# Kernel optimization log

Measured on AMD Instinct MI355X. Metric: run time of the kernel, lower is better.

The kernel has to match this reference:

```python
import jax, jax.numpy as jnp
import numpy as np

EMBED_DIM = 512
NUM_HEADS = 8
HEAD_DIM = EMBED_DIM // NUM_HEADS
B, N, M = 4, 4096, 4096


def setup_inputs() -> dict:
    key = jax.random.key(0)
    ks = jax.random.split(key, 16)
    s = 0.02
    inp = {
        "query": jax.random.normal(ks[0], (B, N, EMBED_DIM), jnp.float32),
        "key": jax.random.normal(ks[1], (B, M, EMBED_DIM), jnp.float32),
        "value": jax.random.normal(ks[2], (B, M, EMBED_DIM), jnp.float32),
        # Linear weights stored as (in, out) so y = x @ W + b (== torch x @ W.T + b)
        "Wq": jax.random.normal(ks[3], (EMBED_DIM, EMBED_DIM), jnp.float32) * s,
        "bq": jnp.zeros((EMBED_DIM,), jnp.float32),
        "Wk": jax.random.normal(ks[4], (EMBED_DIM, EMBED_DIM), jnp.float32) * s,
        "bk": jnp.zeros((EMBED_DIM,), jnp.float32),
        "Wv": jax.random.normal(ks[5], (EMBED_DIM, EMBED_DIM), jnp.float32) * s,
        "bv": jnp.zeros((EMBED_DIM,), jnp.float32),
        # rank expansion MLP acts per-head on head_dim
        "W1": jax.random.normal(ks[6], (HEAD_DIM, HEAD_DIM * 2), jnp.float32) * s,
        "b1": jnp.zeros((HEAD_DIM * 2,), jnp.float32),
        "W2": jax.random.normal(ks[7], (HEAD_DIM * 2, HEAD_DIM), jnp.float32) * s,
        "b2": jnp.zeros((HEAD_DIM,), jnp.float32),
        "Wo": jax.random.normal(ks[8], (EMBED_DIM, EMBED_DIM), jnp.float32) * s,
        "bo": jnp.zeros((EMBED_DIM,), jnp.float32),
    }
    return inp


def reference(query, key, value, Wq, bq, Wk, bk, Wv, bv, W1, b1, W2, b2, Wo, bo):
    b, n, _ = query.shape
    m = key.shape[1]
    H, D = NUM_HEADS, HEAD_DIM
    # ELU+1 feature maps on projected q, k
    q = jax.nn.elu(query @ Wq + bq) + 1.0           # [B,N,E]
    k = jax.nn.elu(key @ Wk + bk) + 1.0             # [B,M,E]
    v = value @ Wv + bv                              # [B,M,E]
    q = q.reshape(b, n, H, D)
    k = k.reshape(b, m, H, D)
    v = v.reshape(b, m, H, D)
    # rank expansion MLP on keys (per head_dim), exact GELU as nn.GELU default
    k_aug = jax.nn.gelu(k @ W1 + b1, approximate=False) @ W2 + b2
    k_aug = jax.nn.elu(k_aug) + 1.0                  # [B,M,H,D]
    # inputs already fp32 (torch .float() casts are identity here)
    k_scaled = k_aug / m                             # normalize over context len
    kv_context = jnp.einsum('bmhd,bmhe->bhde', k_scaled, v)   # [B,H,D,D]
    out = jnp.einsum('bnhd,bhde->bnhe', q, kv_context)        # [B,N,H,D]
    k_sum = k_scaled.sum(axis=1)                      # [B,H,D]
    denom = jnp.einsum('bnhd,bhd->bnh', q, k_sum)     # [B,N,H]
    out = out / jnp.clip(denom, 1e-6, None)[..., None]
    out = jnp.clip(jnp.nan_to_num(out, nan=0.0, posinf=65000.0, neginf=-65000.0),
                   -65000.0, 65000.0)
    out = out.reshape(b, n, H * D)
    return out @ Wo + bo
```

## Files before the change

kernel.cpp:

```cpp
#include <hip/hip_runtime.h>
#include <hip/hip_bf16.h>
#include <cmath>

#define DEV __device__ __forceinline__

typedef __bf16 bf16x8 __attribute__((ext_vector_type(8)));
typedef float f32x4 __attribute__((ext_vector_type(4)));
typedef unsigned int u32;
typedef unsigned short u16;

#define S_VMCNT(N) asm volatile("s_waitcnt vmcnt(" #N ")" ::: "memory")
#define S_LGKM0    asm volatile("s_waitcnt lgkmcnt(0)" ::: "memory")
#define S_FENCE    asm volatile("" ::: "memory")
#define S_BAR      __builtin_amdgcn_s_barrier()

DEV u16 f2bf(float f) {
  union { float f; u32 u; } v;
  v.f = f;
  u32 u = v.u;
  u += 0x7fffu + ((u >> 16) & 1u);
  return (u16)(u >> 16);
}
DEV u32 pk2(float a, float b) {
  union { __hip_bfloat162 h2; u32 u; } v;
  v.h2 = __float22bfloat162_rn(float2{a, b});
  return v.u;
}

DEV void async16(const void* g, void* l) {
  __builtin_amdgcn_global_load_lds((const __attribute__((address_space(1))) u32*)g,
                                   (__attribute__((address_space(3))) u32*)l, 16, 0, 0);
}

DEV int swz(int row, int kq) { return row * 64 + ((kq * 8) ^ ((row & 7) << 3)); }

__global__ __launch_bounds__(256, 2)
void qkv_gemm(const float* __restrict__ qin, const float* __restrict__ kin,
              const float* __restrict__ vin, const u16* __restrict__ WqP,
              const u16* __restrict__ WkP, const u16* __restrict__ WvP,
              const float* __restrict__ bq, const float* __restrict__ bk,
              const float* __restrict__ bv, const u16* __restrict__ W1T,
              const u16* __restrict__ W2T, const float* __restrict__ b1,
              const float* __restrict__ b2, u16* __restrict__ qact,
              u16* __restrict__ vT, u16* __restrict__ kaT, float invM)
{
  __shared__ __align__(16) u16 SB[32768];

  const int z = blockIdx.z;
  const float* Af = z == 0 ? qin : z == 1 ? kin : vin;
  const u16* Bp = z == 0 ? WqP : z == 1 ? WkP : WvP;
  const float* bias = z == 0 ? bq : z == 1 ? bk : bv;

  const int tid = threadIdx.x, wv = tid >> 6, lane = tid & 63;
  const int wr = wv >> 1, wc = wv & 1;
  const int lrow = lane & 15, lq = lane >> 4;
  const long r0 = (long)blockIdx.x * 128;
  const int c0 = blockIdx.y * 128;

  f32x4 acc[4][4] = {};
  float4 rA[2][8];

  auto loadA = [&](float4* dst, int T) {
#pragma unroll
    for (int it = 0; it < 4; ++it) {
      const int s = it * 256 + tid;
      const int row = s >> 3, kq = s & 7;
      const float* g = Af + (r0 + row) * 512 + T * 64 + kq * 8;
      dst[2 * it]     = *(const float4*)g;
      dst[2 * it + 1] = *(const float4*)(g + 4);
    }
  };
  auto cvtStoreA = [&](const float4* src, u16* bufA) {
#pragma unroll
    for (int it = 0; it < 4; ++it) {
      const int s = it * 256 + tid;
      const int row = s >> 3, kq = s & 7;
      union { u32 q[4]; uint4 v; } pk;
      pk.q[0] = pk2(src[2 * it].x, src[2 * it].y);
      pk.q[1] = pk2(src[2 * it].z, src[2 * it].w);
      pk.q[2] = pk2(src[2 * it + 1].x, src[2 * it + 1].y);
      pk.q[3] = pk2(src[2 * it + 1].z, src[2 * it + 1].w);
      *(uint4*)&bufA[swz(row, kq)] = pk.v;
    }
  };
  auto issueB = [&](int T, u16* bufB) {
#pragma unroll
    for (int it = 0; it < 4; ++it) {
      const int sl = it * 256 + wv * 64;
      async16(Bp + ((long)blockIdx.y * 8 + T) * 8192 + (sl + lane) * 8, &bufB[sl * 8]);
    }
  };
  auto computeT = [&](const u16* Ac, const u16* Bc) {
#pragma unroll
    for (int subk = 0; subk < 2; ++subk) {
      bf16x8 af[4], bfr[4];
#pragma unroll
      for (int i = 0; i < 4; ++i)
        af[i] = *(const bf16x8*)&Ac[swz(wr * 64 + i * 16 + lrow, subk * 4 + lq)];
#pragma unroll
      for (int j = 0; j < 4; ++j)
        bfr[j] = *(const bf16x8*)&Bc[swz(wc * 64 + j * 16 + lrow, subk * 4 + lq)];
#pragma unroll
      for (int i = 0; i < 4; ++i)
#pragma unroll
        for (int j = 0; j < 4; ++j)
          acc[i][j] = __builtin_amdgcn_mfma_f32_16x16x32_bf16(af[i], bfr[j], acc[i][j], 0, 0, 0);
    }
  };

  issueB(0, SB + 8192);
  S_FENCE;
  loadA(rA[0], 0);
  loadA(rA[1], 1);
  cvtStoreA(rA[0], SB);
  S_LGKM0;
  S_VMCNT(8);
  S_BAR;

#pragma unroll
  for (int t = 0; t < 8; ++t) {
    const int cur = t & 1, nxt = 1 - cur;
    u16* Ac = SB + cur * 16384;
    u16* Bc = Ac + 8192;
    u16* An = SB + nxt * 16384;
    u16* Bn = An + 8192;
    if (t < 7) issueB(t + 1, Bn);
    S_FENCE;
    if (t < 6) loadA(rA[cur], t + 2);
    if (t < 7) cvtStoreA(rA[nxt], An);
    computeT(Ac, Bc);
    S_LGKM0;
    if (t < 6)       { S_VMCNT(8); }
    else if (t == 6) { S_VMCNT(0); }
    S_BAR;
  }

  if (z == 0) {
#pragma unroll
    for (int i = 0; i < 4; ++i) {
#pragma unroll
      for (int j = 0; j < 4; ++j) {
        const int col = c0 + wc * 64 + j * 16 + lrow;
        const float bvv = bias[col];
#pragma unroll
        for (int p = 0; p < 4; ++p) {
          float o = acc[i][j][p] + bvv;
          o = (o > 0.f) ? (o + 1.f) : __expf(o);
          const long row = r0 + wr * 64 + i * 16 + lq * 4 + p;
          qact[row * 512 + col] = f2bf(o);
        }
      }
    }
  } else if (z == 2) {
    __syncthreads();
    u16* LTv = SB + wv * 4608;
#pragma unroll
    for (int i = 0; i < 4; ++i) {
#pragma unroll
      for (int j = 0; j < 4; ++j) {
        const int col = c0 + wc * 64 + j * 16 + lrow;
        const float bvv = bias[col];
        ushort4 w;
        w.x = f2bf(acc[i][j][0] + bvv);
        w.y = f2bf(acc[i][j][1] + bvv);
        w.z = f2bf(acc[i][j][2] + bvv);
        w.w = f2bf(acc[i][j][3] + bvv);
        *(ushort4*)&LTv[(j * 16 + lrow) * 72 + i * 16 + lq * 4] = w;
      }
    }
    const int b = (int)(r0 >> 12);
    const int h = (c0 + wc * 64) >> 6;
    const int mg0 = (int)(r0 & 4095) + wr * 64;
    __syncthreads();
#pragma unroll
    for (int ps = 0; ps < 8; ++ps) {
      const int e = ps * 8 + (lane >> 3);
      const int mq = (lane & 7) * 8;
      uint4 v = *(const uint4*)&LTv[e * 72 + mq];
      *(uint4*)(vT + (((long)b * 8 + h) * 64 + e) * 4096 + mg0 + mq) = v;
    }
  } else {
    u16* As_k = SB;
    u16* W1p  = SB + 9216;
    u16* W2p  = SB + 18432;
    u16* hid  = SB;
    u16* LT2  = SB;
    const int b   = (int)(r0 >> 12);
    const int m0g = (int)(r0 & 4095);
    const int h0  = c0 >> 6;
    __syncthreads();

    for (int hh = 0; hh < 2; ++hh) {
#pragma unroll
      for (int i = 0; i < 4; ++i) {
        const int c = i * 256 + tid;
        *(uint4*)&W1p[(c >> 3) * 72 + (c & 7) * 8] = *(const uint4*)(W1T + c * 8);
      }
#pragma unroll
      for (int i = 0; i < 4; ++i) {
        const int c = i * 256 + tid;
        *(uint4*)&W2p[(c >> 4) * 136 + (c & 15) * 8] = *(const uint4*)(W2T + c * 8);
      }
      if (wc == hh) {
#pragma unroll
        for (int i = 0; i < 4; ++i)
#pragma unroll
          for (int j = 0; j < 4; ++j) {
            const int col = c0 + wc * 64 + j * 16 + lrow;
            const float bvv = bias[col];
            const int d = j * 16 + lrow;
            const int mb = wr * 64 + i * 16 + lq * 4;
#pragma unroll
            for (int p = 0; p < 4; ++p) {
              float o = acc[i][j][p] + bvv;
              o = (o > 0.f) ? (o + 1.f) : __expf(o);
              As_k[(mb + p) * 72 + d] = f2bf(o);
            }
          }
      }
      __syncthreads();

      const int c0m = (wv >> 1) * 64, mh0 = (wv & 1) * 64;
      f32x4 acc1[4][4] = {};
#pragma unroll
      for (int kt = 0; kt < 2; ++kt) {
        bf16x8 wa[4], kb[4];
#pragma unroll
        for (int i = 0; i < 4; ++i)
          wa[i] = *(const bf16x8*)&W1p[(c0m + i * 16 + lrow) * 72 + kt * 32 + lq * 8];
#pragma unroll
        for (int j = 0; j < 4; ++j)
          kb[j] = *(const bf16x8*)&As_k[(mh0 + j * 16 + lrow) * 72 + kt * 32 + lq * 8];
#pragma unroll
        for (int i = 0; i < 4; ++i)
#pragma unroll
          for (int j = 0; j < 4; ++j)
            acc1[i][j] = __builtin_amdgcn_mfma_f32_16x16x32_bf16(wa[i], kb[j], acc1[i][j], 0, 0, 0);
      }
      __syncthreads();

#pragma unroll
      for (int i = 0; i < 4; ++i) {
        const int cc = c0m + i * 16 + lq * 4;
        float4 bv4 = *(const float4*)(b1 + cc);
#pragma unroll
        for (int j = 0; j < 4; ++j) {
          const int m = mh0 + j * 16 + lrow;
          float x0 = acc1[i][j][0] + bv4.x, x1 = acc1[i][j][1] + bv4.y;
          float x2 = acc1[i][j][2] + bv4.z, x3 = acc1[i][j][3] + bv4.w;
          ushort4 w;
          w.x = f2bf(0.5f * x0 * (1.f + erff(x0 * 0.7071067811865475f)));
          w.y = f2bf(0.5f * x1 * (1.f + erff(x1 * 0.7071067811865475f)));
          w.z = f2bf(0.5f * x2 * (1.f + erff(x2 * 0.7071067811865475f)));
          w.w = f2bf(0.5f * x3 * (1.f + erff(x3 * 0.7071067811865475f)));
          *(ushort4*)&hid[m * 136 + cc] = w;
        }
      }
      __syncthreads();

      const int d0 = (wv >> 1) * 32, mh2 = (wv & 1) * 64;
      f32x4 acc2[4][2] = {};
#pragma unroll
      for (int kt = 0; kt < 4; ++kt) {
        bf16x8 wa2[2], hb[4];
#pragma unroll
        for (int i = 0; i < 2; ++i)
          wa2[i] = *(const bf16x8*)&W2p[(d0 + i * 16 + lrow) * 136 + kt * 32 + lq * 8];
#pragma unroll
        for (int j = 0; j < 4; ++j)
          hb[j] = *(const bf16x8*)&hid[(mh2 + j * 16 + lrow) * 136 + kt * 32 + lq * 8];
#pragma unroll
        for (int j = 0; j < 4; ++j)
#pragma unroll
          for (int i = 0; i < 2; ++i)
            acc2[j][i] = __builtin_amdgcn_mfma_f32_16x16x32_bf16(hb[j], wa2[i], acc2[j][i], 0, 0, 0);
      }
      __syncthreads();

#pragma unroll
      for (int i = 0; i < 2; ++i) {
        const int d = d0 + i * 16 + lrow;
        const float bd = b2[d];
#pragma unroll
        for (int j = 0; j < 4; ++j) {
          const int ml = mh2 + j * 16 + lq * 4;
          ushort4 w;
#pragma unroll
          for (int p = 0; p < 4; ++p) {
            float v = acc2[j][i][p] + bd;
            v = ((v > 0.f) ? (v + 1.f) : __expf(v)) * invM;
            ((u16*)&w)[p] = f2bf(v);
          }
          *(ushort4*)&LT2[d * 136 + ml] = w;
        }
      }
      __syncthreads();

      const int bh2 = b * 8 + h0 + hh;
#pragma unroll
      for (int it = 0; it < 4; ++it) {
        const int c = it * 256 + tid;
        const int d = c >> 4, mq = (c & 15) * 8;
        uint4 v = *(const uint4*)&LT2[d * 136 + mq];
        *(uint4*)(kaT + ((long)bh2 * 64 + d) * 4096 + m0g + mq) = v;
      }
      __syncthreads();
    }
  }
}

__global__ __launch_bounds__(256, 2)
void out_gemm(const u16* __restrict__ A, const u16* __restrict__ Bt,
              const float* __restrict__ bias, float* __restrict__ Y)
{
  __shared__ __align__(16) u16 SB[32768];
  const int tid = threadIdx.x, wv = tid >> 6, lane = tid & 63;
  const int wr = wv >> 1, wc = wv & 1;
  const int lrow = lane & 15, lq = lane >> 4;
  const long r0 = (long)blockIdx.x * 128;
  const int c0 = blockIdx.y * 128;

  auto stage = [&](int T, u16* buf) {
#pragma unroll
    for (int it = 0; it < 4; ++it) {
      const int sl = it * 256 + wv * 64;
      async16(A  + ((long)blockIdx.x * 8 + T) * 8192 + (sl + lane) * 8, &buf[sl * 8]);
      async16(Bt + ((long)blockIdx.y * 8 + T) * 8192 + (sl + lane) * 8, &buf[8192 + sl * 8]);
    }
  };

  f32x4 acc[4][4] = {};
  stage(0, SB);
  S_VMCNT(0);
  S_BAR;

#pragma unroll
  for (int t = 0; t < 8; ++t) {
    const int cur = t & 1, nxt = 1 - cur;
    if (t < 7) stage(t + 1, SB + nxt * 16384);
    const u16* Ac = SB + cur * 16384;
    const u16* Bc = Ac + 8192;
#pragma unroll
    for (int subk = 0; subk < 2; ++subk) {
      bf16x8 af[4], bfr[4];
#pragma unroll
      for (int i = 0; i < 4; ++i)
        af[i] = *(const bf16x8*)&Ac[swz(wr * 64 + i * 16 + lrow, subk * 4 + lq)];
#pragma unroll
      for (int j = 0; j < 4; ++j)
        bfr[j] = *(const bf16x8*)&Bc[swz(wc * 64 + j * 16 + lrow, subk * 4 + lq)];
#pragma unroll
      for (int i = 0; i < 4; ++i)
#pragma unroll
        for (int j = 0; j < 4; ++j)
          acc[i][j] = __builtin_amdgcn_mfma_f32_16x16x32_bf16(af[i], bfr[j], acc[i][j], 0, 0, 0);
    }
    S_LGKM0;
    if (t < 7) { S_VMCNT(0); }
    S_BAR;
  }
#pragma unroll
  for (int i = 0; i < 4; ++i) {
#pragma unroll
    for (int j = 0; j < 4; ++j) {
      const int col = c0 + wc * 64 + j * 16 + lrow;
      const float bv = bias[col];
#pragma unroll
      for (int p = 0; p < 4; ++p) {
        const long row = r0 + wr * 64 + i * 16 + lq * 4 + p;
        Y[row * 512 + col] = acc[i][j][p] + bv;
      }
    }
  }
}

struct TArgs {
  const float* src[6];
  u16* dst[6];
  int K[6];
  int N[6];
};
__global__ __launch_bounds__(256)
void transpose_w(TArgs a)
{
  const int m = blockIdx.z;
  const int K = a.K[m], N = a.N[m];
  const int kt = blockIdx.y * 64, nt = blockIdx.x * 64;
  if (kt >= K || nt >= N) return;
  const float* src = a.src[m];
  u16* dst = a.dst[m];
  __shared__ u16 t[64][72];
  const int tx = threadIdx.x & 15, ty = threadIdx.x >> 4;
#pragma unroll
  for (int rr = 0; rr < 64; rr += 16) {
    const int k = kt + ty + rr;
    float4 v = *(const float4*)(src + (long)k * N + nt + tx * 4);
    t[tx * 4 + 0][ty + rr] = f2bf(v.x);
    t[tx * 4 + 1][ty + rr] = f2bf(v.y);
    t[tx * 4 + 2][ty + rr] = f2bf(v.z);
    t[tx * 4 + 3][ty + rr] = f2bf(v.w);
  }
  __syncthreads();
  if (m < 4) {
    const int ktile = kt >> 6;
#pragma unroll
    for (int it = 0; it < 2; ++it) {
      const int s = threadIdx.x + it * 256;
      const int r = s >> 3, c = (s & 7) * 8;
      const int n = nt + r;
      const int colblk = n >> 7, cl = n & 127;
      ushort4 u0 = *(ushort4*)&t[r][c];
      ushort4 u1 = *(ushort4*)&t[r][c + 4];
      u16* d = dst + ((long)colblk * 8 + ktile) * 8192 + cl * 64 + (c ^ ((cl & 7) << 3));
      *(ushort4*)d = u0;
      *(ushort4*)(d + 4) = u1;
    }
  } else {
#pragma unroll
    for (int it = 0; it < 2; ++it) {
      const int s = threadIdx.x + it * 256;
      const int r = s >> 3, c = (s & 7) * 8;
      ushort4 u0 = *(ushort4*)&t[r][c];
      ushort4 u1 = *(ushort4*)&t[r][c + 4];
      *(ushort4*)(dst + (long)(nt + r) * K + kt + c) = u0;
      *(ushort4*)(dst + (long)(nt + r) * K + kt + c + 4) = u1;
    }
  }
}

__global__ __launch_bounds__(256, 2)
void kv_gemm(const u16* __restrict__ kaT, const u16* __restrict__ vT,
             float* __restrict__ kvp, float* __restrict__ ksp)
{
  const int sp = blockIdx.x;
  const int bh = blockIdx.y;
  __shared__ __align__(16) u16 SB[32768];
  const int tid = threadIdx.x, wv = tid >> 6, lane = tid & 63;
  const int lrow = lane & 15, lq = lane >> 4;
  f32x4 acc[4][4] = {};
  f32x4 accs[4] = {};
  bf16x8 ones;
#pragma unroll
  for (int z = 0; z < 8; ++z) ones[z] = (__bf16)1.0f;
  const long base = (long)bh * 64 * 4096;

#pragma unroll
  for (int ph = 0; ph < 2; ++ph) {
    const int m0 = sp * 256 + ph * 128;
#pragma unroll
    for (int i = 0; i < 4; ++i) {
      const int s = (wv * 4 + i) * 64 + lane;
      const int chunk = s >> 8, row = (s >> 2) & 63, part = s & 3;
      const long g = base + (long)row * 4096 + m0 + chunk * 32 + part * 8;
      async16(kaT + g, &SB[ph * 16384 + (wv * 4 + i) * 512]);
      async16(vT + g, &SB[ph * 16384 + 8192 + (wv * 4 + i) * 512]);
    }
    S_FENCE;
  }

#pragma unroll
  for (int ph = 0; ph < 2; ++ph) {
    if (ph == 0) { S_VMCNT(8); } else { S_VMCNT(0); }
    const u16* As = SB + ph * 16384;
    const u16* Bs = As + 8192;
    bf16x8 af[4], bfr[4];
#pragma unroll
    for (int i = 0; i < 4; ++i)
      af[i] = *(const bf16x8*)&As[wv * 2048 + (i * 16 + lrow) * 32 + lq * 8];
#pragma unroll
    for (int j = 0; j < 4; ++j)
      bfr[j] = *(const bf16x8*)&Bs[wv * 2048 + (j * 16 + lrow) * 32 + lq * 8];
#pragma unroll
    for (int i = 0; i < 4; ++i) {
#pragma unroll
      for (int j = 0; j < 4; ++j)
        acc[i][j] = __builtin_amdgcn_mfma_f32_16x16x32_bf16(af[i], bfr[j], acc[i][j], 0, 0, 0);
      accs[i] = __builtin_amdgcn_mfma_f32_16x16x32_bf16(af[i], ones, accs[i], 0, 0, 0);
    }
  }

  float* red = (float*)SB;
  float* ksr = red + 64 * 68;
  for (int w = 0; w < 4; ++w) {
    __syncthreads();
    if (wv == w) {
#pragma unroll
      for (int i = 0; i < 4; ++i) {
#pragma unroll
        for (int j = 0; j < 4; ++j) {
          const int e = j * 16 + lrow, dd = i * 16 + lq * 4;
          float* p = &red[e * 68 + dd];
          if (w == 0) { p[0] = acc[i][j][0]; p[1] = acc[i][j][1]; p[2] = acc[i][j][2]; p[3] = acc[i][j][3]; }
          else        { p[0] += acc[i][j][0]; p[1] += acc[i][j][1]; p[2] += acc[i][j][2]; p[3] += acc[i][j][3]; }
        }
        if (lrow == 0) {
          const int dd = i * 16 + lq * 4;
#pragma unroll
          for (int p2 = 0; p2 < 4; ++p2) {
            if (w == 0) ksr[dd + p2] = accs[i][p2];
            else        ksr[dd + p2] += accs[i][p2];
          }
        }
      }
    }
  }
  __syncthreads();
  float* kvo = kvp + ((long)sp * 32 + bh) * 4096;
  for (int s = tid; s < 4096; s += 256) kvo[s] = red[(s >> 6) * 68 + (s & 63)];
  if (tid < 64) ksp[(sp * 32 + bh) * 64 + tid] = ksr[tid];
}

__global__ __launch_bounds__(256)
void kv_reduce(const float* __restrict__ kvp, const float* __restrict__ ksp,
               u16* __restrict__ kvT, u16* __restrict__ ksumT)
{
  const int bh = blockIdx.x;
  const int t = threadIdx.x;
  const int s0 = blockIdx.y * 512;
#pragma unroll
  for (int i = 0; i < 2; ++i) {
    const int s = s0 + i * 256 + t;
    float v = 0.f;
#pragma unroll
    for (int sp = 0; sp < 16; ++sp) v += kvp[((long)sp * 32 + bh) * 4096 + s];
    kvT[(long)bh * 4096 + s] = f2bf(v);
  }
  if (blockIdx.y == 0 && t < 64) {
    float v = 0.f;
#pragma unroll
    for (int sp = 0; sp < 16; ++sp) v += ksp[(sp * 32 + bh) * 64 + t];
    ksumT[bh * 64 + t] = f2bf(v);
  }
}

__global__ __launch_bounds__(256)
void attn_mfma(const u16* __restrict__ q, const u16* __restrict__ kvT,
               const u16* __restrict__ ksumT, u16* __restrict__ attn)
{
  __shared__ u16 SB[17408];
  const int tid = threadIdx.x, wv = tid >> 6, lane = tid & 63;
  const int lrow = lane & 15, lq = lane >> 4;
  const int n0 = blockIdx.x * 256;
  const int bh = blockIdx.y, b = bh >> 3, h = bh & 7;
  u16* As = SB;

#pragma unroll
  for (int half = 0; half < 2; ++half)
#pragma unroll
    for (int i = 0; i < 4; ++i) {
      const int s = (wv * 4 + i) * 64 + lane;
      async16(q + ((long)(b * 4096 + n0 + (s >> 2))) * 512 + h * 64 + half * 32 + (s & 3) * 8,
              &As[half * 8192 + (wv * 4 + i) * 512]);
    }
  bf16x8 bfr[2][4], ks[2];
#pragma unroll
  for (int half = 0; half < 2; ++half) {
#pragma unroll
    for (int j = 0; j < 4; ++j)
      bfr[half][j] = *(const bf16x8*)(kvT + ((long)bh * 64 + j * 16 + lrow) * 64 + half * 32 + lq * 8);
    ks[half] = *(const bf16x8*)(ksumT + bh * 64 + half * 32 + lq * 8);
  }
  __syncthreads();

  f32x4 acc[4][4] = {};
  f32x4 accd[4] = {};
#pragma unroll
  for (int half = 0; half < 2; ++half) {
    bf16x8 af[4];
#pragma unroll
    for (int i = 0; i < 4; ++i)
      af[i] = *(const bf16x8*)&As[half * 8192 + (wv * 64 + i * 16 + lrow) * 32 + lq * 8];
#pragma unroll
    for (int i = 0; i < 4; ++i) {
#pragma unroll
      for (int j = 0; j < 4; ++j)
        acc[i][j] = __builtin_amdgcn_mfma_f32_16x16x32_bf16(af[i], bfr[half][j], acc[i][j], 0, 0, 0);
      accd[i] = __builtin_amdgcn_mfma_f32_16x16x32_bf16(af[i], ks[half], accd[i], 0, 0, 0);
    }
  }
  __syncthreads();

  u16* LT = SB;
#pragma unroll
  for (int i = 0; i < 4; ++i) {
    float dinv[4];
#pragma unroll
    for (int p = 0; p < 4; ++p) dinv[p] = 1.f / fmaxf(accd[i][p], 1e-6f);
#pragma unroll
    for (int j = 0; j < 4; ++j) {
      const int e = j * 16 + lrow;
      const int nl0 = i * 16 + lq * 4;
      ushort4 w;
      float x0 = acc[i][j][0] * dinv[0], x1 = acc[i][j][1] * dinv[1];
      float x2 = acc[i][j][2] * dinv[2], x3 = acc[i][j][3] * dinv[3];
      if (!(x0 == x0)) x0 = 0.f;
      if (!(x1 == x1)) x1 = 0.f;
      if (!(x2 == x2)) x2 = 0.f;
      if (!(x3 == x3)) x3 = 0.f;
      w.x = f2bf(fminf(65000.f, fmaxf(-65000.f, x0)));
      w.y = f2bf(fminf(65000.f, fmaxf(-65000.f, x1)));
      w.z = f2bf(fminf(65000.f, fmaxf(-65000.f, x2)));
      w.w = f2bf(fminf(65000.f, fmaxf(-65000.f, x3)));
      *(ushort4*)&LT[wv * 4352 + e * 68 + nl0] = w;
    }
  }
  __syncthreads();
#pragma unroll
  for (int it = 0; it < 8; ++it) {
    const int c = it * 256 + tid;
    const int n = c & 255, ec = c >> 8;
    const int wr2 = n >> 6, nl = n & 63;
    ushort4 w0, w1;
    w0.x = LT[wr2 * 4352 + (ec * 8 + 0) * 68 + nl];
    w0.y = LT[wr2 * 4352 + (ec * 8 + 1) * 68 + nl];
    w0.z = LT[wr2 * 4352 + (ec * 8 + 2) * 68 + nl];
    w0.w = LT[wr2 * 4352 + (ec * 8 + 3) * 68 + nl];
    w1.x = LT[wr2 * 4352 + (ec * 8 + 4) * 68 + nl];
    w1.y = LT[wr2 * 4352 + (ec * 8 + 5) * 68 + nl];
    w1.z = LT[wr2 * 4352 + (ec * 8 + 6) * 68 + nl];
    w1.w = LT[wr2 * 4352 + (ec * 8 + 7) * 68 + nl];
    const int ng = b * 4096 + n0 + n;
    const int rowblk = ng >> 7, rl = ng & 127;
    u16* dst = attn + ((long)rowblk * 8 + h) * 8192 + rl * 64 + ((ec * 8) ^ ((rl & 7) << 3));
    *(ushort4*)dst = w0;
    *(ushort4*)(dst + 4) = w1;
  }
}

static constexpr long U = 8388608;

extern "C" void kernel_launch(void* const* d_in, const int* in_sizes, int n_in,
                              void* d_out, int out_size, void* d_ws, size_t ws_size,
                              hipStream_t stream)
{
  const float* query = (const float*)d_in[0];
  const float* key   = (const float*)d_in[1];
  const float* value = (const float*)d_in[2];
  const float* Wq = (const float*)d_in[3];
  const float* bq = (const float*)d_in[4];
  const float* Wk = (const float*)d_in[5];
  const float* bk = (const float*)d_in[6];
  const float* Wv = (const float*)d_in[7];
  const float* bv = (const float*)d_in[8];
  const float* W1 = (const float*)d_in[9];
  const float* b1 = (const float*)d_in[10];
  const float* W2 = (const float*)d_in[11];
  const float* b2 = (const float*)d_in[12];
  const float* Wo = (const float*)d_in[13];
  const float* bo = (const float*)d_in[14];

  u16* wsh = (u16*)d_ws;
  u16* qact = wsh;
  u16* vT   = wsh + 2 * U;
  u16* kaT  = wsh + 3 * U;
  u16* attn = wsh + 4 * U;

  float* fp  = (float*)(wsh + 5 * U);
  float* kvp = fp;
  float* ksp = fp + 2097152;
  u16* kvTg   = (u16*)(fp + 2129920);
  u16* ksumTg = kvTg + 131072;
  u16* wtb = ksumTg + 2048;
  u16* WqT = wtb;
  u16* WkT = wtb + 262144;
  u16* WvT = wtb + 524288;
  u16* WoT = wtb + 786432;
  u16* W1T = wtb + 1048576;
  u16* W2T = wtb + 1056768;

  dim3 blk(256);
  const float invM = 1.f / 4096.f;

  TArgs ta;
  ta.src[0] = Wq; ta.dst[0] = WqT; ta.K[0] = 512; ta.N[0] = 512;
  ta.src[1] = Wk; ta.dst[1] = WkT; ta.K[1] = 512; ta.N[1] = 512;
  ta.src[2] = Wv; ta.dst[2] = WvT; ta.K[2] = 512; ta.N[2] = 512;
  ta.src[3] = Wo; ta.dst[3] = WoT; ta.K[3] = 512; ta.N[3] = 512;
  ta.src[4] = W1; ta.dst[4] = W1T; ta.K[4] = 64;  ta.N[4] = 128;
  ta.src[5] = W2; ta.dst[5] = W2T; ta.K[5] = 128; ta.N[5] = 64;
  transpose_w<<<dim3(8, 8, 6), blk, 0, stream>>>(ta);

  qkv_gemm<<<dim3(128, 4, 3), blk, 0, stream>>>(query, key, value, WqT, WkT, WvT,
                                                bq, bk, bv, W1T, W2T, b1, b2,
                                                qact, vT, kaT, invM);
  kv_gemm<<<dim3(16, 32), blk, 0, stream>>>(kaT, vT, kvp, ksp);
  kv_reduce<<<dim3(32, 8), blk, 0, stream>>>(kvp, ksp, kvTg, ksumTg);
  attn_mfma<<<dim3(16, 32), blk, 0, stream>>>(qact, kvTg, ksumTg, attn);
  out_gemm<<<dim3(128, 4), blk, 0, stream>>>(attn, WoT, bo, (float*)d_out);
}
```

Baseline: 251.7 us.

## Process both heads of key MLP in one pass, reading weights from global

```diff
diff --git a/kernel.cpp b/kernel.cpp
--- a/kernel.cpp
+++ b/kernel.cpp
@@ -181,130 +181,116 @@
     }
   } else {
     u16* As_k = SB;
-    u16* W1p  = SB + 9216;
-    u16* W2p  = SB + 18432;
     u16* hid  = SB;
     u16* LT2  = SB;
     const int b   = (int)(r0 >> 12);
     const int m0g = (int)(r0 & 4095);
     const int h0  = c0 >> 6;
-    __syncthreads();
-
-    for (int hh = 0; hh < 2; ++hh) {
-#pragma unroll
-      for (int i = 0; i < 4; ++i) {
-        const int c = i * 256 + tid;
-        *(uint4*)&W1p[(c >> 3) * 72 + (c & 7) * 8] = *(const uint4*)(W1T + c * 8);
-      }
-#pragma unroll
-      for (int i = 0; i < 4; ++i) {
-        const int c = i * 256 + tid;
-        *(uint4*)&W2p[(c >> 4) * 136 + (c & 15) * 8] = *(const uint4*)(W2T + c * 8);
-      }
-      if (wc == hh) {
+    const int hw  = wv & 1;
+    const int mh  = (wv >> 1) * 64;
+    __syncthreads();
+
+#pragma unroll
+    for (int i = 0; i < 4; ++i)
+#pragma unroll
+      for (int j = 0; j < 4; ++j) {
+        const int col = c0 + wc * 64 + j * 16 + lrow;
+        const float bvv = bias[col];
+        const int d = j * 16 + lrow;
+        const int mb = wr * 64 + i * 16 + lq * 4;
+#pragma unroll
+        for (int p = 0; p < 4; ++p) {
+          float o = acc[i][j][p] + bvv;
+          o = (o > 0.f) ? (o + 1.f) : __expf(o);
+          As_k[wc * 9216 + (mb + p) * 72 + d] = f2bf(o);
+        }
+      }
+    __syncthreads();
+
+    f32x4 acc1[8][4] = {};
+#pragma unroll
+    for (int kt = 0; kt < 2; ++kt) {
+      bf16x8 wa[8], kb[4];
+#pragma unroll
+      for (int i = 0; i < 8; ++i)
+        wa[i] = *(const bf16x8*)(W1T + (i * 16 + lrow) * 64 + kt * 32 + lq * 8);
+#pragma unroll
+      for (int j = 0; j < 4; ++j)
+        kb[j] = *(const bf16x8*)&As_k[hw * 9216 + (mh + j * 16 + lrow) * 72 + kt * 32 + lq * 8];
+#pragma unroll
+      for (int i = 0; i < 8; ++i)
+#pragma unroll
+        for (int j = 0; j < 4; ++j)
+          acc1[i][j] = __builtin_amdgcn_mfma_f32_16x16x32_bf16(wa[i], kb[j], acc1[i][j], 0, 0, 0);
+    }
+    __syncthreads();
+
+#pragma unroll
+    for (int i = 0; i < 8; ++i) {
+      const int cc = i * 16 + lq * 4;
+      float4 bv4 = *(const float4*)(b1 + cc);
+#pragma unroll
+      for (int j = 0; j < 4; ++j) {
+        const int m = mh + j * 16 + lrow;
+        float x0 = acc1[i][j][0] + bv4.x, x1 = acc1[i][j][1] + bv4.y;
+        float x2 = acc1[i][j][2] + bv4.z, x3 = acc1[i][j][3] + bv4.w;
+        ushort4 w;
+        w.x = f2bf(0.5f * x0 * (1.f + erff(x0 * 0.7071067811865475f)));
+        w.y = f2bf(0.5f * x1 * (1.f + erff(x1 * 0.7071067811865475f)));
+        w.z = f2bf(0.5f * x2 * (1.f + erff(x2 * 0.7071067811865475f)));
+        w.w = f2bf(0.5f * x3 * (1.f + erff(x3 * 0.7071067811865475f)));
+        const int off = hw * 16384 + m * 128 + ((((cc >> 3) ^ (m & 7)) << 3) | (cc & 7));
+        *(ushort4*)&hid[off] = w;
+      }
+    }
+    __syncthreads();
+
+    f32x4 acc2[4][4] = {};
+#pragma unroll
+    for (int kt = 0; kt < 4; ++kt) {
+      bf16x8 wa2[4], hb[4];
+#pragma unroll
+      for (int i = 0; i < 4; ++i)
+        wa2[i] = *(const bf16x8*)(W2T + (i * 16 + lrow) * 128 + kt * 32 + lq * 8);
+#pragma unroll
+      for (int j = 0; j < 4; ++j) {
+        const int m = mh + j * 16 + lrow;
+        const int k0 = kt * 32 + lq * 8;
+        hb[j] = *(const bf16x8*)&hid[hw * 16384 + m * 128 + (((k0 >> 3) ^ (m & 7)) << 3)];
+      }
+#pragma unroll
+      for (int j = 0; j < 4; ++j)
 #pragma unroll
         for (int i = 0; i < 4; ++i)
-#pragma unroll
-          for (int j = 0; j < 4; ++j) {
-            const int col = c0 + wc * 64 + j * 16 + lrow;
-            const float bvv = bias[col];
-            const int d = j * 16 + lrow;
-            const int mb = wr * 64 + i * 16 + lq * 4;
-#pragma unroll
-            for (int p = 0; p < 4; ++p) {
-              float o = acc[i][j][p] + bvv;
-              o = (o > 0.f) ? (o + 1.f) : __expf(o);
-              As_k[(mb + p) * 72 + d] = f2bf(o);
-            }
-          }
-      }
-      __syncthreads();
-
-      const int c0m = (wv >> 1) * 64, mh0 = (wv & 1) * 64;
-      f32x4 acc1[4][4] = {};
-#pragma unroll
-      for (int kt = 0; kt < 2; ++kt) {
-        bf16x8 wa[4], kb[4];
-#pragma unroll
-        for (int i = 0; i < 4; ++i)
-          wa[i] = *(const bf16x8*)&W1p[(c0m + i * 16 + lrow) * 72 + kt * 32 + lq * 8];
-#pragma unroll
-        for (int j = 0; j < 4; ++j)
-          kb[j] = *(const bf16x8*)&As_k[(mh0 + j * 16 + lrow) * 72 + kt * 32 + lq * 8];
-#pragma unroll
-        for (int i = 0; i < 4; ++i)
-#pragma unroll
-          for (int j = 0; j < 4; ++j)
-            acc1[i][j] = __builtin_amdgcn_mfma_f32_16x16x32_bf16(wa[i], kb[j], acc1[i][j], 0, 0, 0);
-      }
-      __syncthreads();
-
-#pragma unroll
-      for (int i = 0; i < 4; ++i) {
-        const int cc = c0m + i * 16 + lq * 4;
-        float4 bv4 = *(const float4*)(b1 + cc);
-#pragma unroll
-        for (int j = 0; j < 4; ++j) {
-          const int m = mh0 + j * 16 + lrow;
-          float x0 = acc1[i][j][0] + bv4.x, x1 = acc1[i][j][1] + bv4.y;
-          float x2 = acc1[i][j][2] + bv4.z, x3 = acc1[i][j][3] + bv4.w;
-          ushort4 w;
-          w.x = f2bf(0.5f * x0 * (1.f + erff(x0 * 0.7071067811865475f)));
-          w.y = f2bf(0.5f * x1 * (1.f + erff(x1 * 0.7071067811865475f)));
-          w.z = f2bf(0.5f * x2 * (1.f + erff(x2 * 0.7071067811865475f)));
-          w.w = f2bf(0.5f * x3 * (1.f + erff(x3 * 0.7071067811865475f)));
-          *(ushort4*)&hid[m * 136 + cc] = w;
+          acc2[j][i] = __builtin_amdgcn_mfma_f32_16x16x32_bf16(hb[j], wa2[i], acc2[j][i], 0, 0, 0);
+    }
+    __syncthreads();
+
+#pragma unroll
+    for (int i = 0; i < 4; ++i) {
+      const int d = i * 16 + lrow;
+      const float bd = b2[d];
+#pragma unroll
+      for (int j = 0; j < 4; ++j) {
+        const int ml = mh + j * 16 + lq * 4;
+        ushort4 w;
+#pragma unroll
+        for (int p = 0; p < 4; ++p) {
+          float v = acc2[j][i][p] + bd;
+          v = ((v > 0.f) ? (v + 1.f) : __expf(v)) * invM;
+          ((u16*)&w)[p] = f2bf(v);
         }
-      }
-      __syncthreads();
-
-      const int d0 = (wv >> 1) * 32, mh2 = (wv & 1) * 64;
-      f32x4 acc2[4][2] = {};
-#pragma unroll
-      for (int kt = 0; kt < 4; ++kt) {
-        bf16x8 wa2[2], hb[4];
-#pragma unroll
-        for (int i = 0; i < 2; ++i)
-          wa2[i] = *(const bf16x8*)&W2p[(d0 + i * 16 + lrow) * 136 + kt * 32 + lq * 8];
-#pragma unroll
-        for (int j = 0; j < 4; ++j)
-          hb[j] = *(const bf16x8*)&hid[(mh2 + j * 16 + lrow) * 136 + kt * 32 + lq * 8];
-#pragma unroll
-        for (int j = 0; j < 4; ++j)
-#pragma unroll
-          for (int i = 0; i < 2; ++i)
-            acc2[j][i] = __builtin_amdgcn_mfma_f32_16x16x32_bf16(hb[j], wa2[i], acc2[j][i], 0, 0, 0);
-      }
-      __syncthreads();
-
-#pragma unroll
-      for (int i = 0; i < 2; ++i) {
-        const int d = d0 + i * 16 + lrow;
-        const float bd = b2[d];
-#pragma unroll
-        for (int j = 0; j < 4; ++j) {
-          const int ml = mh2 + j * 16 + lq * 4;
-          ushort4 w;
-#pragma unroll
-          for (int p = 0; p < 4; ++p) {
-            float v = acc2[j][i][p] + bd;
-            v = ((v > 0.f) ? (v + 1.f) : __expf(v)) * invM;
-            ((u16*)&w)[p] = f2bf(v);
-          }
-          *(ushort4*)&LT2[d * 136 + ml] = w;
-        }
-      }
-      __syncthreads();
-
-      const int bh2 = b * 8 + h0 + hh;
-#pragma unroll
-      for (int it = 0; it < 4; ++it) {
-        const int c = it * 256 + tid;
-        const int d = c >> 4, mq = (c & 15) * 8;
-        uint4 v = *(const uint4*)&LT2[d * 136 + mq];
-        *(uint4*)(kaT + ((long)bh2 * 64 + d) * 4096 + m0g + mq) = v;
-      }
-      __syncthreads();
+        *(ushort4*)&LT2[(hw * 64 + d) * 136 + ml] = w;
+      }
+    }
+    __syncthreads();
+
+#pragma unroll
+    for (int it = 0; it < 8; ++it) {
+      const int u = it * 256 + tid;
+      const int mo = u & 15, hd = u >> 4;
+      uint4 v = *(const uint4*)&LT2[hd * 136 + mo * 8];
+      *(uint4*)(kaT + ((long)(b * 8 + h0 + (hd >> 6)) * 64 + (hd & 63)) * 4096 + m0g + mo * 8) = v;
     }
   }
 }
```

New measurement: 369.8 us. +47.0%, slower.

## Restructure key MLP epilogue with swizzled LDS and fewer barriers

Applied to the files above, without the earlier changes.

```diff
diff --git a/kernel.cpp b/kernel.cpp
--- a/kernel.cpp
+++ b/kernel.cpp
@@ -152,7 +152,6 @@
       }
     }
   } else if (z == 2) {
-    __syncthreads();
     u16* LTv = SB + wv * 4608;
 #pragma unroll
     for (int i = 0; i < 4; ++i) {
@@ -181,63 +180,50 @@
     }
   } else {
     u16* As_k = SB;
-    u16* W1p  = SB + 9216;
-    u16* W2p  = SB + 18432;
-    u16* hid  = SB;
-    u16* LT2  = SB;
+    u16* hid  = SB + 16384;
     const int b   = (int)(r0 >> 12);
     const int m0g = (int)(r0 & 4095);
     const int h0  = c0 >> 6;
+
+#pragma unroll
+    for (int i = 0; i < 4; ++i)
+#pragma unroll
+      for (int j = 0; j < 4; ++j) {
+        const int col = c0 + wc * 64 + j * 16 + lrow;
+        const float bvv = bias[col];
+        const int d = j * 16 + lrow;
+#pragma unroll
+        for (int p = 0; p < 4; ++p) {
+          const int m = wr * 64 + i * 16 + lq * 4 + p;
+          float o = acc[i][j][p] + bvv;
+          o = (o > 0.f) ? (o + 1.f) : __expf(o);
+          As_k[wc * 8192 + m * 64 + ((((d >> 3) ^ (m & 7)) << 3) | (d & 7))] = f2bf(o);
+        }
+      }
     __syncthreads();
 
+    const int c0m = (wv >> 1) * 64, mh0 = (wv & 1) * 64;
+    const int d0  = (wv >> 1) * 32, mh2 = (wv & 1) * 64;
+
     for (int hh = 0; hh < 2; ++hh) {
-#pragma unroll
-      for (int i = 0; i < 4; ++i) {
-        const int c = i * 256 + tid;
-        *(uint4*)&W1p[(c >> 3) * 72 + (c & 7) * 8] = *(const uint4*)(W1T + c * 8);
-      }
-#pragma unroll
-      for (int i = 0; i < 4; ++i) {
-        const int c = i * 256 + tid;
-        *(uint4*)&W2p[(c >> 4) * 136 + (c & 15) * 8] = *(const uint4*)(W2T + c * 8);
-      }
-      if (wc == hh) {
-#pragma unroll
-        for (int i = 0; i < 4; ++i)
-#pragma unroll
-          for (int j = 0; j < 4; ++j) {
-            const int col = c0 + wc * 64 + j * 16 + lrow;
-            const float bvv = bias[col];
-            const int d = j * 16 + lrow;
-            const int mb = wr * 64 + i * 16 + lq * 4;
-#pragma unroll
-            for (int p = 0; p < 4; ++p) {
-              float o = acc[i][j][p] + bvv;
-              o = (o > 0.f) ? (o + 1.f) : __expf(o);
-              As_k[(mb + p) * 72 + d] = f2bf(o);
-            }
-          }
-      }
-      __syncthreads();
-
-      const int c0m = (wv >> 1) * 64, mh0 = (wv & 1) * 64;
       f32x4 acc1[4][4] = {};
 #pragma unroll
       for (int kt = 0; kt < 2; ++kt) {
         bf16x8 wa[4], kb[4];
 #pragma unroll
         for (int i = 0; i < 4; ++i)
-          wa[i] = *(const bf16x8*)&W1p[(c0m + i * 16 + lrow) * 72 + kt * 32 + lq * 8];
-#pragma unroll
-        for (int j = 0; j < 4; ++j)
-          kb[j] = *(const bf16x8*)&As_k[(mh0 + j * 16 + lrow) * 72 + kt * 32 + lq * 8];
+          wa[i] = *(const bf16x8*)(W1T + (c0m + i * 16 + lrow) * 64 + kt * 32 + lq * 8);
+#pragma unroll
+        for (int j = 0; j < 4; ++j) {
+          const int m = mh0 + j * 16 + lrow;
+          kb[j] = *(const bf16x8*)&As_k[hh * 8192 + m * 64 + (((kt * 4 + lq) ^ (m & 7)) << 3)];
+        }
 #pragma unroll
         for (int i = 0; i < 4; ++i)
 #pragma unroll
           for (int j = 0; j < 4; ++j)
             acc1[i][j] = __builtin_amdgcn_mfma_f32_16x16x32_bf16(wa[i], kb[j], acc1[i][j], 0, 0, 0);
       }
-      __syncthreads();
 
 #pragma unroll
       for (int i = 0; i < 4; ++i) {
@@ -253,30 +239,31 @@
           w.y = f2bf(0.5f * x1 * (1.f + erff(x1 * 0.7071067811865475f)));
           w.z = f2bf(0.5f * x2 * (1.f + erff(x2 * 0.7071067811865475f)));
           w.w = f2bf(0.5f * x3 * (1.f + erff(x3 * 0.7071067811865475f)));
-          *(ushort4*)&hid[m * 136 + cc] = w;
+          *(ushort4*)&hid[m * 128 + ((((cc >> 3) ^ (m & 7)) << 3) | (cc & 7))] = w;
         }
       }
       __syncthreads();
 
-      const int d0 = (wv >> 1) * 32, mh2 = (wv & 1) * 64;
       f32x4 acc2[4][2] = {};
 #pragma unroll
       for (int kt = 0; kt < 4; ++kt) {
         bf16x8 wa2[2], hb[4];
 #pragma unroll
         for (int i = 0; i < 2; ++i)
-          wa2[i] = *(const bf16x8*)&W2p[(d0 + i * 16 + lrow) * 136 + kt * 32 + lq * 8];
-#pragma unroll
-        for (int j = 0; j < 4; ++j)
-          hb[j] = *(const bf16x8*)&hid[(mh2 + j * 16 + lrow) * 136 + kt * 32 + lq * 8];
+          wa2[i] = *(const bf16x8*)(W2T + (d0 + i * 16 + lrow) * 128 + kt * 32 + lq * 8);
+#pragma unroll
+        for (int j = 0; j < 4; ++j) {
+          const int m = mh2 + j * 16 + lrow;
+          hb[j] = *(const bf16x8*)&hid[m * 128 + (((kt * 4 + lq) ^ (m & 7)) << 3)];
+        }
 #pragma unroll
         for (int j = 0; j < 4; ++j)
 #pragma unroll
           for (int i = 0; i < 2; ++i)
             acc2[j][i] = __builtin_amdgcn_mfma_f32_16x16x32_bf16(hb[j], wa2[i], acc2[j][i], 0, 0, 0);
       }
-      __syncthreads();
-
+
+      u16* LT2 = SB + hh * 8192;
 #pragma unroll
       for (int i = 0; i < 2; ++i) {
         const int d = d0 + i * 16 + lrow;
@@ -291,7 +278,7 @@
             v = ((v > 0.f) ? (v + 1.f) : __expf(v)) * invM;
             ((u16*)&w)[p] = f2bf(v);
           }
-          *(ushort4*)&LT2[d * 136 + ml] = w;
+          *(ushort4*)&LT2[d * 128 + ((((ml >> 3) ^ (d & 7)) << 3) | (ml & 7))] = w;
         }
       }
       __syncthreads();
@@ -299,12 +286,11 @@
       const int bh2 = b * 8 + h0 + hh;
 #pragma unroll
       for (int it = 0; it < 4; ++it) {
-        const int c = it * 256 + tid;
-        const int d = c >> 4, mq = (c & 15) * 8;
-        uint4 v = *(const uint4*)&LT2[d * 136 + mq];
-        *(uint4*)(kaT + ((long)bh2 * 64 + d) * 4096 + m0g + mq) = v;
-      }
-      __syncthreads();
+        const int u = it * 256 + tid;
+        const int mo = u & 15, hd = u >> 4;
+        uint4 v = *(const uint4*)&LT2[hd * 128 + ((mo ^ (hd & 7)) << 3)];
+        *(uint4*)(kaT + ((long)bh2 * 64 + hd) * 4096 + m0g + mo * 8) = v;
+      }
     }
   }
 }
```

Result: no change. 249.3 us (-0.9%).
